# Kernel optimization log

Measured on AMD Instinct MI355X. Metric: run time of the kernel, lower is better.

The kernel has to match this reference:

```python
import jax, jax.numpy as jnp
import numpy as np

VOCAB = 25
HIDDEN = 512
B, S = 64, 2048


def setup_inputs() -> dict:
    key = jax.random.key(0)
    ks = jax.random.split(key, 8)
    tokens = jax.random.randint(ks[0], (B, S), 0, VOCAB)
    lengths = jax.random.randint(ks[1], (B,), 1, S + 1)  # pack_padded requires length >= 1
    k = 1.0 / np.sqrt(HIDDEN)
    u = lambda kk, shp: jax.random.uniform(kk, shp, jnp.float32, -k, k)
    return {
        "tokens": tokens,
        "lengths": lengths,
        "W_ih": u(ks[2], (4 * HIDDEN, VOCAB)),   # gate order i,f,g,o (PyTorch)
        "W_hh": u(ks[3], (4 * HIDDEN, HIDDEN)),
        "b_ih": u(ks[4], (4 * HIDDEN,)),
        "b_hh": u(ks[5], (4 * HIDDEN,)),
        "fc_w": u(ks[6], (1, HIDDEN)),
        "fc_b": u(ks[7], (1,)),
    }


def _lstm_last_hidden(x, lengths, W_ih, W_hh, b_ih, b_hh):
    # x: [B,S,V] one-hot; returns h at each sequence's last valid step (packed-LSTM semantics)
    b, s, _ = x.shape
    h0 = jnp.zeros((b, HIDDEN), x.dtype)
    c0 = jnp.zeros((b, HIDDEN), x.dtype)
    # precompute input projections for all steps: [S,B,4H]
    xg = jnp.einsum('bsv,gv->sbg', x, W_ih) + b_ih + b_hh

    def step(carry, inp):
        h, c = carry
        xt, t = inp
        gates = xt + h @ W_hh.T
        i, f, g, o = jnp.split(gates, 4, axis=-1)
        i = jax.nn.sigmoid(i); f = jax.nn.sigmoid(f)
        g = jnp.tanh(g); o = jax.nn.sigmoid(o)
        c_new = f * c + i * g
        h_new = o * jnp.tanh(c_new)
        m = (t < lengths)[:, None]  # freeze state past sequence end
        return (jnp.where(m, h_new, h), jnp.where(m, c_new, c)), None

    (h, _), _ = jax.lax.scan(step, (h0, c0), (xg, jnp.arange(s)))
    return h


def reference(tokens, lengths, W_ih, W_hh, b_ih, b_hh, fc_w, fc_b):
    # sort by length descending, like the torch forward (output stays in sorted order)
    order = jnp.argsort(-lengths)
    toks = tokens[order]
    lens = lengths[order]
    x = jax.nn.one_hot(toks, VOCAB, dtype=jnp.float32)  # fused one-hot (replaces python loop)
    h = _lstm_last_hidden(x, lens, W_ih, W_hh, b_ih, b_hh)
    return h @ fc_w.T + fc_b  # [B,1]
```

## Files before the change

### kernel.cpp

```cpp
#include <hip/hip_runtime.h>


#define VOCAB 25
#define HIDDEN 512
#define BATCH 64
#define SEQ 2048
#define GB 16
#define NG 4
#define WPG 16
#define HSL 32
#define RWG 128
#define NTHREADS 256
#define HGQ (GB * HIDDEN / 2)

typedef short s16x8 __attribute__((ext_vector_type(8)));
typedef float f32x4 __attribute__((ext_vector_type(4)));

__device__ inline unsigned short f2bf(float x) {
  unsigned u = __float_as_uint(x);
  u += 0x7fffu + ((u >> 16) & 1u);
  return (unsigned short)(u >> 16);
}
__device__ inline float sigf(float x) { return 1.0f / (1.0f + __expf(-x)); }
__device__ inline float tanh_fast(float x) { return 2.0f / (1.0f + __expf(-2.0f * x)) - 1.0f; }

__global__ void prep_kernel(unsigned long long* hg, float* out) {
  const int i = blockIdx.x * blockDim.x + threadIdx.x;
  const int n = blockDim.x * gridDim.x;
  for (int k = i; k < 2 * NG * HGQ; k += n) hg[k] = 0ull;
  if (i < BATCH) out[i] = 0.f;
}

__global__ __launch_bounds__(NTHREADS, 1) void lstm_persistent(
    const int* __restrict__ tokens, const int* __restrict__ lengths,
    const float* __restrict__ W_ih, const float* __restrict__ W_hh,
    const float* __restrict__ b_ih, const float* __restrict__ b_hh,
    const float* __restrict__ fc_w, const float* __restrict__ fc_b,
    float* __restrict__ out, unsigned long long* hg) {
  const int tid = threadIdx.x;
  const int bid = blockIdx.x;
  const int x = bid & 7;
  const int g = x >> 1;
  const int w = ((bid >> 3) << 1) | (x & 1);

  __shared__ __align__(16) unsigned short hbuf[GB][HIDDEN + 8];
  __shared__ float gatesb[GB][RWG + 5];
  __shared__ float xgt[VOCAB][RWG + 5];
  __shared__ int lenAll[BATCH];
  __shared__ int order_[BATCH];
  __shared__ int gIdx[GB];
  __shared__ int gLen[GB];

  if (tid < BATCH) lenAll[tid] = lengths[tid];
  __syncthreads();
  if (tid < BATCH) {
    const int L = lenAll[tid];
    int r = 0;
    for (int j = 0; j < BATCH; ++j) {
      const int lj = lenAll[j];
      r += ((lj > L) || (lj == L && j < tid)) ? 1 : 0;
    }
    order_[r] = tid;
  }
  __syncthreads();
  if (tid < GB) {
    const int oi = order_[g * GB + tid];
    gIdx[tid] = oi;
    gLen[tid] = lenAll[oi];
  }
  for (int i = tid; i < GB * (HIDDEN + 8); i += NTHREADS)
    ((unsigned short*)hbuf)[i] = 0;
  for (int i = tid; i < VOCAB * RWG; i += NTHREADS) {
    const int v = i / RWG, rl = i % RWG;
    const int rg = (rl >> 5) * HIDDEN + w * HSL + (rl & 31);
    xgt[v][rl] = W_ih[rg * VOCAB + v] + b_ih[rg] + b_hh[rg];
  }
  __syncthreads();

  const int T = gLen[0];
  const int lane = tid & 63;
  const int wv = tid >> 6;
  const int m16 = lane & 15;
  const int quad = lane >> 4;

  s16x8 Bf[2][16];
#pragma unroll
  for (int nti = 0; nti < 2; ++nti) {
    const int nt = wv + 4 * nti;
    const int rl = nt * 16 + m16;
    const int rg = (rl >> 5) * HIDDEN + w * HSL + (rl & 31);
    const float* wr = W_hh + (size_t)rg * HIDDEN;
#pragma unroll
    for (int kt = 0; kt < 16; ++kt) {
      const float* p = wr + kt * 32 + quad * 8;
#pragma unroll
      for (int e = 0; e < 8; ++e) Bf[nti][kt][e] = (short)f2bf(p[e]);
    }
  }

  const int cb = tid >> 4;
  const int cs = tid & 15;
  const int jj0 = 2 * cs, jj1 = 2 * cs + 1;
  const int myLen = gLen[cb];
  const int* tokRow = tokens + (size_t)gIdx[cb] * SEQ;
  unsigned long long* const base0 = hg + (size_t)g * HGQ;
  unsigned long long* const base1 = hg + (size_t)(NG + g) * HGQ;

  float c0 = 0.f, c1 = 0.f, h0 = 0.f, h1 = 0.f;

  for (int t = 0; t < T; ++t) {
    const int tok = tokRow[t];

    if (t > 0) {
      const unsigned long long* src = ((t & 1) ? base1 : base0) + tid;
      unsigned long long q[16];
      for (;;) {
        bool ok = true;
#pragma unroll
        for (int r = 0; r < 16; ++r)
          q[r] = __hip_atomic_load(src + r * 256, __ATOMIC_RELAXED,
                                   __HIP_MEMORY_SCOPE_AGENT);
#pragma unroll
        for (int r = 0; r < 16; ++r) ok &= ((unsigned)(q[r] >> 32) == (unsigned)t);
        if (ok) break;
      }
#pragma unroll
      for (int r = 0; r < 16; ++r)
        *(unsigned*)&hbuf[cb][r * 32 + jj0] = (unsigned)q[r];
    }
    __syncthreads();

    f32x4 acc0a = {0.f, 0.f, 0.f, 0.f}, acc0b = {0.f, 0.f, 0.f, 0.f};
    f32x4 acc1a = {0.f, 0.f, 0.f, 0.f}, acc1b = {0.f, 0.f, 0.f, 0.f};
#pragma unroll
    for (int kt = 0; kt < 16; kt += 2) {
      const s16x8 A0 = *(const s16x8*)&hbuf[m16][kt * 32 + quad * 8];
      const s16x8 A1 = *(const s16x8*)&hbuf[m16][(kt + 1) * 32 + quad * 8];
      acc0a = __builtin_amdgcn_mfma_f32_16x16x32_bf16(A0, Bf[0][kt], acc0a, 0, 0, 0);
      acc1a = __builtin_amdgcn_mfma_f32_16x16x32_bf16(A0, Bf[1][kt], acc1a, 0, 0, 0);
      acc0b = __builtin_amdgcn_mfma_f32_16x16x32_bf16(A1, Bf[0][kt + 1], acc0b, 0, 0, 0);
      acc1b = __builtin_amdgcn_mfma_f32_16x16x32_bf16(A1, Bf[1][kt + 1], acc1b, 0, 0, 0);
    }
    const f32x4 acc0 = acc0a + acc0b;
    const f32x4 acc1 = acc1a + acc1b;
#pragma unroll
    for (int v = 0; v < 4; ++v) {
      gatesb[quad * 4 + v][wv * 16 + m16] = acc0[v];
      gatesb[quad * 4 + v][(wv + 4) * 16 + m16] = acc1[v];
    }
    __syncthreads();

    const float pi0 = gatesb[cb][jj0] + xgt[tok][jj0];
    const float pf0 = gatesb[cb][32 + jj0] + xgt[tok][32 + jj0];
    const float pg0 = gatesb[cb][64 + jj0] + xgt[tok][64 + jj0];
    const float po0 = gatesb[cb][96 + jj0] + xgt[tok][96 + jj0];
    const float pi1 = gatesb[cb][jj1] + xgt[tok][jj1];
    const float pf1 = gatesb[cb][32 + jj1] + xgt[tok][32 + jj1];
    const float pg1 = gatesb[cb][64 + jj1] + xgt[tok][64 + jj1];
    const float po1 = gatesb[cb][96 + jj1] + xgt[tok][96 + jj1];
    if (t < myLen) {
      const float i0 = sigf(pi0), f0 = sigf(pf0), g0 = tanh_fast(pg0), o0 = sigf(po0);
      c0 = f0 * c0 + i0 * g0;
      h0 = o0 * tanh_fast(c0);
      const float i1 = sigf(pi1), f1 = sigf(pf1), g1 = tanh_fast(pg1), o1 = sigf(po1);
      c1 = f1 * c1 + i1 * g1;
      h1 = o1 * tanh_fast(c1);
    }
    if (t + 1 < T) {
      const unsigned payload = (unsigned)f2bf(h0) | ((unsigned)f2bf(h1) << 16);
      const unsigned long long qv = ((unsigned long long)(unsigned)(t + 1) << 32) | payload;
      unsigned long long* hp = (((t + 1) & 1) ? base1 : base0) + w * 256 + tid;
      __hip_atomic_store(hp, qv, __ATOMIC_RELAXED, __HIP_MEMORY_SCOPE_AGENT);
    }
  }

  float part = h0 * fc_w[w * HSL + jj0] + h1 * fc_w[w * HSL + jj1];
  part += __shfl_down(part, 8, 16);
  part += __shfl_down(part, 4, 16);
  part += __shfl_down(part, 2, 16);
  part += __shfl_down(part, 1, 16);
  if (cs == 0) {
    if (w == 0) part += fc_b[0];
    atomicAdd(&out[g * GB + cb], part);
  }
}

extern "C" void kernel_launch(void* const* d_in, const int* in_sizes, int n_in,
                              void* d_out, int out_size, void* d_ws, size_t ws_size,
                              hipStream_t stream) {
  (void)in_sizes; (void)n_in; (void)out_size; (void)ws_size;
  const int* tokens = (const int*)d_in[0];
  const int* lengths = (const int*)d_in[1];
  const float* W_ih = (const float*)d_in[2];
  const float* W_hh = (const float*)d_in[3];
  const float* b_ih = (const float*)d_in[4];
  const float* b_hh = (const float*)d_in[5];
  const float* fc_w = (const float*)d_in[6];
  const float* fc_b = (const float*)d_in[7];
  float* out = (float*)d_out;
  unsigned long long* hglob = (unsigned long long*)d_ws;

  prep_kernel<<<32, 256, 0, stream>>>(hglob, out);
  lstm_persistent<<<64, NTHREADS, 0, stream>>>(tokens, lengths, W_ih, W_hh, b_ih, b_hh,
                                               fc_w, fc_b, out, hglob);
}
```

Baseline: 5.560 ms.

## Split each batch group into two interleaved half-groups to overlap exchange latency

Each block's 16-sequence group is split into two 8-sequence subgroups (P and Q, alternating by length rank), which are processed alternately within each timestep. While one subgroup computes, the other's hidden-state exchange is issued early through inline-asm global loads, hiding cross-block synchronisation latency. The exchange format packs a 16-bit tag with each bf16 value, halving the payload per word. The MFMA tiles are now half empty (only 8 of 16 rows are valid), and the extra __syncthreads and the more complex tag polling add overhead.

```diff
diff --git a/kernel.cpp b/kernel.cpp
--- a/kernel.cpp
+++ b/kernel.cpp
@@ -5,16 +5,16 @@
 #define HIDDEN 512
 #define BATCH 64
 #define SEQ 2048
-#define GB 16
-#define NG 4
+#define GBH 8
 #define WPG 16
 #define HSL 32
 #define RWG 128
 #define NTHREADS 256
-#define HGQ (GB * HIDDEN / 2)
+#define GQW 2048
 
 typedef short s16x8 __attribute__((ext_vector_type(8)));
 typedef float f32x4 __attribute__((ext_vector_type(4)));
+typedef unsigned long long ull;
 
 __device__ inline unsigned short f2bf(float x) {
   unsigned u = __float_as_uint(x);
@@ -24,10 +24,35 @@
 __device__ inline float sigf(float x) { return 1.0f / (1.0f + __expf(-x)); }
 __device__ inline float tanh_fast(float x) { return 2.0f / (1.0f + __expf(-2.0f * x)) - 1.0f; }
 
-__global__ void prep_kernel(unsigned long long* hg, float* out) {
+#define PREFETCH8(QARR, QB)                                                  \
+  asm volatile(                                                              \
+      "global_load_dwordx2 %[a0], %[v0], %[b] sc0 sc1\n\t"                   \
+      "global_load_dwordx2 %[a1], %[v0], %[b] offset:1024 sc0 sc1\n\t"       \
+      "global_load_dwordx2 %[a2], %[v0], %[b] offset:2048 sc0 sc1\n\t"       \
+      "global_load_dwordx2 %[a3], %[v0], %[b] offset:3072 sc0 sc1\n\t"       \
+      "global_load_dwordx2 %[a4], %[v1], %[b] sc0 sc1\n\t"                   \
+      "global_load_dwordx2 %[a5], %[v1], %[b] offset:1024 sc0 sc1\n\t"       \
+      "global_load_dwordx2 %[a6], %[v1], %[b] offset:2048 sc0 sc1\n\t"       \
+      "global_load_dwordx2 %[a7], %[v1], %[b] offset:3072 sc0 sc1"           \
+      : [a0] "=&v"(QARR[0]), [a1] "=&v"(QARR[1]), [a2] "=&v"(QARR[2]),       \
+        [a3] "=&v"(QARR[3]), [a4] "=&v"(QARR[4]), [a5] "=&v"(QARR[5]),       \
+        [a6] "=&v"(QARR[6]), [a7] "=&v"(QARR[7])                             \
+      : [v0] "v"(vo0), [v1] "v"(vo1), [b] "s"(QB)                            \
+      : "memory")
+
+#define TAGOK8(QARR, TU, OK)                                                 \
+  do {                                                                       \
+    OK = true;                                                               \
+    _Pragma("unroll") for (int r_ = 0; r_ < 8; ++r_) {                       \
+      OK &= (((unsigned)(QARR[r_] >> 16) & 0xFFFFu) == (TU));                \
+      OK &= (((unsigned)(QARR[r_] >> 48)) == (TU));                          \
+    }                                                                        \
+  } while (0)
+
+__global__ void prep_kernel(ull* hg, float* out) {
   const int i = blockIdx.x * blockDim.x + threadIdx.x;
   const int n = blockDim.x * gridDim.x;
-  for (int k = i; k < 2 * NG * HGQ; k += n) hg[k] = 0ull;
+  for (int k = i; k < 16 * GQW; k += n) hg[k] = 0ull;
   if (i < BATCH) out[i] = 0.f;
 }
 
@@ -36,40 +61,44 @@
     const float* __restrict__ W_ih, const float* __restrict__ W_hh,
     const float* __restrict__ b_ih, const float* __restrict__ b_hh,
     const float* __restrict__ fc_w, const float* __restrict__ fc_b,
-    float* __restrict__ out, unsigned long long* hg) {
+    float* __restrict__ out, ull* hg) {
   const int tid = threadIdx.x;
   const int bid = blockIdx.x;
-  const int x = bid & 7;
-  const int g = x >> 1;
-  const int w = ((bid >> 3) << 1) | (x & 1);
-
-  __shared__ __align__(16) unsigned short hbuf[GB][HIDDEN + 8];
-  __shared__ float gatesb[GB][RWG + 5];
+  const int xr = bid & 7;
+  const int pair = xr >> 1;
+  const int w = ((bid >> 3) << 1) | (xr & 1);
+
+  __shared__ __align__(16) unsigned short hbufP[16][HIDDEN + 8];
+  __shared__ __align__(16) unsigned short hbufQ[16][HIDDEN + 8];
+  __shared__ float gatesbP[GBH][RWG + 5];
+  __shared__ float gatesbQ[GBH][RWG + 5];
   __shared__ float xgt[VOCAB][RWG + 5];
   __shared__ int lenAll[BATCH];
   __shared__ int order_[BATCH];
-  __shared__ int gIdx[GB];
-  __shared__ int gLen[GB];
+  __shared__ int gIdxP[GBH], gLenP[GBH], gIdxQ[GBH], gLenQ[GBH];
 
   if (tid < BATCH) lenAll[tid] = lengths[tid];
   __syncthreads();
   if (tid < BATCH) {
     const int L = lenAll[tid];
     int r = 0;
-    for (int j = 0; j < BATCH; ++j) {
-      const int lj = lenAll[j];
-      r += ((lj > L) || (lj == L && j < tid)) ? 1 : 0;
+    for (int jx = 0; jx < BATCH; ++jx) {
+      const int lj = lenAll[jx];
+      r += ((lj > L) || (lj == L && jx < tid)) ? 1 : 0;
     }
     order_[r] = tid;
   }
   __syncthreads();
-  if (tid < GB) {
-    const int oi = order_[g * GB + tid];
-    gIdx[tid] = oi;
-    gLen[tid] = lenAll[oi];
-  }
-  for (int i = tid; i < GB * (HIDDEN + 8); i += NTHREADS)
-    ((unsigned short*)hbuf)[i] = 0;
+  if (tid < GBH) {
+    const int rp = pair * 16 + 2 * tid;
+    const int op = order_[rp], oq = order_[rp + 1];
+    gIdxP[tid] = op; gLenP[tid] = lenAll[op];
+    gIdxQ[tid] = oq; gLenQ[tid] = lenAll[oq];
+  }
+  for (int i = tid; i < 16 * (HIDDEN + 8); i += NTHREADS) {
+    ((unsigned short*)hbufP)[i] = 0;
+    ((unsigned short*)hbufQ)[i] = 0;
+  }
   for (int i = tid; i < VOCAB * RWG; i += NTHREADS) {
     const int v = i / RWG, rl = i % RWG;
     const int rg = (rl >> 5) * HIDDEN + w * HSL + (rl & 31);
@@ -77,7 +106,8 @@
   }
   __syncthreads();
 
-  const int T = gLen[0];
+  const int TP = gLenP[0];
+  const int TQ = gLenQ[0];
   const int lane = tid & 63;
   const int wv = tid >> 6;
   const int m16 = lane & 15;
@@ -98,90 +128,197 @@
     }
   }
 
-  const int cb = tid >> 4;
-  const int cs = tid & 15;
-  const int jj0 = 2 * cs, jj1 = 2 * cs + 1;
-  const int myLen = gLen[cb];
-  const int* tokRow = tokens + (size_t)gIdx[cb] * SEQ;
-  unsigned long long* const base0 = hg + (size_t)g * HGQ;
-  unsigned long long* const base1 = hg + (size_t)(NG + g) * HGQ;
-
-  float c0 = 0.f, c1 = 0.f, h0 = 0.f, h1 = 0.f;
-
-  for (int t = 0; t < T; ++t) {
-    const int tok = tokRow[t];
+  const int cb = tid >> 5;
+  const int j = tid & 31;
+  const int h128 = tid >> 7;
+  const int cbq = (tid >> 4) & 7;
+  const int pp = tid & 15;
+  const int myLenP = gLenP[cb], myLenQ = gLenQ[cb];
+  const int* tokRowP = tokens + (size_t)gIdxP[cb] * SEQ;
+  const int* tokRowQ = tokens + (size_t)gIdxQ[cb] * SEQ;
+
+  ull* const bP0 = hg + (size_t)(2 * pair) * GQW;
+  ull* const bP1 = hg + (size_t)(8 + 2 * pair) * GQW;
+  ull* const bQ0 = hg + (size_t)(2 * pair + 1) * GQW;
+  ull* const bQ1 = hg + (size_t)(8 + 2 * pair + 1) * GQW;
+
+  const unsigned vo0 = (unsigned)(h128 * 8192 + (cbq * 16 + pp) * 8);
+  const unsigned vo1 = vo0 + 4096;
+  const int sIdx = w * 256 + cb * 32 + j;
+
+  ull qP[8], qQ[8];
+  float cP = 0.f, hP = 0.f, cQ = 0.f, hQ = 0.f;
+
+  for (int t = 0; t < TP; ++t) {
+    const unsigned tu = (unsigned)t;
 
     if (t > 0) {
-      const unsigned long long* src = ((t & 1) ? base1 : base0) + tid;
-      unsigned long long q[16];
-      for (;;) {
-        bool ok = true;
-#pragma unroll
-        for (int r = 0; r < 16; ++r)
-          q[r] = __hip_atomic_load(src + r * 256, __ATOMIC_RELAXED,
-                                   __HIP_MEMORY_SCOPE_AGENT);
-#pragma unroll
-        for (int r = 0; r < 16; ++r) ok &= ((unsigned)(q[r] >> 32) == (unsigned)t);
-        if (ok) break;
-      }
-#pragma unroll
-      for (int r = 0; r < 16; ++r)
-        *(unsigned*)&hbuf[cb][r * 32 + jj0] = (unsigned)q[r];
+      asm volatile("s_waitcnt vmcnt(1)" ::: "memory");
+      __builtin_amdgcn_sched_barrier(0);
+      bool ok;
+      TAGOK8(qP, tu, ok);
+      if (!ok) {
+        const ull* src = ((t & 1) ? bP1 : bP0) + h128 * 1024 + cbq * 16 + pp;
+        for (;;) {
+#pragma unroll
+          for (int r = 0; r < 8; ++r)
+            qP[r] = __hip_atomic_load(src + r * 128, __ATOMIC_RELAXED,
+                                      __HIP_MEMORY_SCOPE_AGENT);
+          TAGOK8(qP, tu, ok);
+          if (ok) break;
+        }
+      }
+#pragma unroll
+      for (int r = 0; r < 8; ++r) {
+        const unsigned lo = (unsigned)qP[r] & 0xFFFFu;
+        const unsigned hi = (unsigned)(qP[r] >> 32) & 0xFFFFu;
+        *(unsigned*)&hbufP[cbq][(h128 * 8 + r) * 32 + 2 * pp] = lo | (hi << 16);
+      }
     }
     __syncthreads();
-
-    f32x4 acc0a = {0.f, 0.f, 0.f, 0.f}, acc0b = {0.f, 0.f, 0.f, 0.f};
-    f32x4 acc1a = {0.f, 0.f, 0.f, 0.f}, acc1b = {0.f, 0.f, 0.f, 0.f};
-#pragma unroll
-    for (int kt = 0; kt < 16; kt += 2) {
-      const s16x8 A0 = *(const s16x8*)&hbuf[m16][kt * 32 + quad * 8];
-      const s16x8 A1 = *(const s16x8*)&hbuf[m16][(kt + 1) * 32 + quad * 8];
-      acc0a = __builtin_amdgcn_mfma_f32_16x16x32_bf16(A0, Bf[0][kt], acc0a, 0, 0, 0);
-      acc1a = __builtin_amdgcn_mfma_f32_16x16x32_bf16(A0, Bf[1][kt], acc1a, 0, 0, 0);
-      acc0b = __builtin_amdgcn_mfma_f32_16x16x32_bf16(A1, Bf[0][kt + 1], acc0b, 0, 0, 0);
-      acc1b = __builtin_amdgcn_mfma_f32_16x16x32_bf16(A1, Bf[1][kt + 1], acc1b, 0, 0, 0);
-    }
-    const f32x4 acc0 = acc0a + acc0b;
-    const f32x4 acc1 = acc1a + acc1b;
-#pragma unroll
-    for (int v = 0; v < 4; ++v) {
-      gatesb[quad * 4 + v][wv * 16 + m16] = acc0[v];
-      gatesb[quad * 4 + v][(wv + 4) * 16 + m16] = acc1[v];
+    const int tokP = tokRowP[t];
+    {
+      f32x4 a0a = {0.f,0.f,0.f,0.f}, a0b = {0.f,0.f,0.f,0.f};
+      f32x4 a1a = {0.f,0.f,0.f,0.f}, a1b = {0.f,0.f,0.f,0.f};
+#pragma unroll
+      for (int kt = 0; kt < 16; kt += 2) {
+        const s16x8 A0 = *(const s16x8*)&hbufP[m16][kt * 32 + quad * 8];
+        const s16x8 A1 = *(const s16x8*)&hbufP[m16][(kt + 1) * 32 + quad * 8];
+        a0a = __builtin_amdgcn_mfma_f32_16x16x32_bf16(A0, Bf[0][kt], a0a, 0, 0, 0);
+        a1a = __builtin_amdgcn_mfma_f32_16x16x32_bf16(A0, Bf[1][kt], a1a, 0, 0, 0);
+        a0b = __builtin_amdgcn_mfma_f32_16x16x32_bf16(A1, Bf[0][kt + 1], a0b, 0, 0, 0);
+        a1b = __builtin_amdgcn_mfma_f32_16x16x32_bf16(A1, Bf[1][kt + 1], a1b, 0, 0, 0);
+      }
+      const f32x4 ac0 = a0a + a0b, ac1 = a1a + a1b;
+      if (quad < 2) {
+#pragma unroll
+        for (int v = 0; v < 4; ++v) {
+          gatesbP[quad * 4 + v][wv * 16 + m16] = ac0[v];
+          gatesbP[quad * 4 + v][(wv + 4) * 16 + m16] = ac1[v];
+        }
+      }
     }
     __syncthreads();
-
-    const float pi0 = gatesb[cb][jj0] + xgt[tok][jj0];
-    const float pf0 = gatesb[cb][32 + jj0] + xgt[tok][32 + jj0];
-    const float pg0 = gatesb[cb][64 + jj0] + xgt[tok][64 + jj0];
-    const float po0 = gatesb[cb][96 + jj0] + xgt[tok][96 + jj0];
-    const float pi1 = gatesb[cb][jj1] + xgt[tok][jj1];
-    const float pf1 = gatesb[cb][32 + jj1] + xgt[tok][32 + jj1];
-    const float pg1 = gatesb[cb][64 + jj1] + xgt[tok][64 + jj1];
-    const float po1 = gatesb[cb][96 + jj1] + xgt[tok][96 + jj1];
-    if (t < myLen) {
-      const float i0 = sigf(pi0), f0 = sigf(pf0), g0 = tanh_fast(pg0), o0 = sigf(po0);
-      c0 = f0 * c0 + i0 * g0;
-      h0 = o0 * tanh_fast(c0);
-      const float i1 = sigf(pi1), f1 = sigf(pf1), g1 = tanh_fast(pg1), o1 = sigf(po1);
-      c1 = f1 * c1 + i1 * g1;
-      h1 = o1 * tanh_fast(c1);
-    }
-    if (t + 1 < T) {
-      const unsigned payload = (unsigned)f2bf(h0) | ((unsigned)f2bf(h1) << 16);
-      const unsigned long long qv = ((unsigned long long)(unsigned)(t + 1) << 32) | payload;
-      unsigned long long* hp = (((t + 1) & 1) ? base1 : base0) + w * 256 + tid;
-      __hip_atomic_store(hp, qv, __ATOMIC_RELAXED, __HIP_MEMORY_SCOPE_AGENT);
-    }
-  }
-
-  float part = h0 * fc_w[w * HSL + jj0] + h1 * fc_w[w * HSL + jj1];
-  part += __shfl_down(part, 8, 16);
-  part += __shfl_down(part, 4, 16);
-  part += __shfl_down(part, 2, 16);
-  part += __shfl_down(part, 1, 16);
-  if (cs == 0) {
-    if (w == 0) part += fc_b[0];
-    atomicAdd(&out[g * GB + cb], part);
+    if (t > 0 && t < TQ) {
+      const ull* qb = (t & 1) ? bQ1 : bQ0;
+      PREFETCH8(qQ, qb);
+    }
+    {
+      const float pi = gatesbP[cb][j] + xgt[tokP][j];
+      const float pf = gatesbP[cb][32 + j] + xgt[tokP][32 + j];
+      const float pg = gatesbP[cb][64 + j] + xgt[tokP][64 + j];
+      const float po = gatesbP[cb][96 + j] + xgt[tokP][96 + j];
+      if (t < myLenP) {
+        const float ii = sigf(pi), ff = sigf(pf), gg = tanh_fast(pg), oo = sigf(po);
+        cP = ff * cP + ii * gg;
+        hP = oo * tanh_fast(cP);
+      }
+      if (t + 1 < TP) {
+        unsigned* dst = (unsigned*)(((t + 1) & 1) ? bP1 : bP0) + sIdx;
+        __hip_atomic_store(dst, ((unsigned)(t + 1) << 16) | (unsigned)f2bf(hP),
+                           __ATOMIC_RELAXED, __HIP_MEMORY_SCOPE_AGENT);
+      }
+    }
+
+    if (t < TQ) {
+      if (t > 0) {
+        asm volatile("s_waitcnt vmcnt(1)" ::: "memory");
+        __builtin_amdgcn_sched_barrier(0);
+        bool ok;
+        TAGOK8(qQ, tu, ok);
+        if (!ok) {
+          const ull* src = ((t & 1) ? bQ1 : bQ0) + h128 * 1024 + cbq * 16 + pp;
+          for (;;) {
+#pragma unroll
+            for (int r = 0; r < 8; ++r)
+              qQ[r] = __hip_atomic_load(src + r * 128, __ATOMIC_RELAXED,
+                                        __HIP_MEMORY_SCOPE_AGENT);
+            TAGOK8(qQ, tu, ok);
+            if (ok) break;
+          }
+        }
+#pragma unroll
+        for (int r = 0; r < 8; ++r) {
+          const unsigned lo = (unsigned)qQ[r] & 0xFFFFu;
+          const unsigned hi = (unsigned)(qQ[r] >> 32) & 0xFFFFu;
+          *(unsigned*)&hbufQ[cbq][(h128 * 8 + r) * 32 + 2 * pp] = lo | (hi << 16);
+        }
+      }
+      __syncthreads();
+      const int tokQ = tokRowQ[t];
+      {
+        f32x4 a0a = {0.f,0.f,0.f,0.f}, a0b = {0.f,0.f,0.f,0.f};
+        f32x4 a1a = {0.f,0.f,0.f,0.f}, a1b = {0.f,0.f,0.f,0.f};
+#pragma unroll
+        for (int kt = 0; kt < 16; kt += 2) {
+          const s16x8 A0 = *(const s16x8*)&hbufQ[m16][kt * 32 + quad * 8];
+          const s16x8 A1 = *(const s16x8*)&hbufQ[m16][(kt + 1) * 32 + quad * 8];
+          a0a = __builtin_amdgcn_mfma_f32_16x16x32_bf16(A0, Bf[0][kt], a0a, 0, 0, 0);
+          a1a = __builtin_amdgcn_mfma_f32_16x16x32_bf16(A0, Bf[1][kt], a1a, 0, 0, 0);
+          a0b = __builtin_amdgcn_mfma_f32_16x16x32_bf16(A1, Bf[0][kt + 1], a0b, 0, 0, 0);
+          a1b = __builtin_amdgcn_mfma_f32_16x16x32_bf16(A1, Bf[1][kt + 1], a1b, 0, 0, 0);
+        }
+        const f32x4 ac0 = a0a + a0b, ac1 = a1a + a1b;
+        if (quad < 2) {
+#pragma unroll
+          for (int v = 0; v < 4; ++v) {
+            gatesbQ[quad * 4 + v][wv * 16 + m16] = ac0[v];
+            gatesbQ[quad * 4 + v][(wv + 4) * 16 + m16] = ac1[v];
+          }
+        }
+      }
+      __syncthreads();
+      if (t + 1 < TP) {
+        const ull* qb = ((t + 1) & 1) ? bP1 : bP0;
+        PREFETCH8(qP, qb);
+      }
+      {
+        const float pi = gatesbQ[cb][j] + xgt[tokQ][j];
+        const float pf = gatesbQ[cb][32 + j] + xgt[tokQ][32 + j];
+        const float pg = gatesbQ[cb][64 + j] + xgt[tokQ][64 + j];
+        const float po = gatesbQ[cb][96 + j] + xgt[tokQ][96 + j];
+        if (t < myLenQ) {
+          const float ii = sigf(pi), ff = sigf(pf), gg = tanh_fast(pg), oo = sigf(po);
+          cQ = ff * cQ + ii * gg;
+          hQ = oo * tanh_fast(cQ);
+        }
+        if (t + 1 < TQ) {
+          unsigned* dst = (unsigned*)(((t + 1) & 1) ? bQ1 : bQ0) + sIdx;
+          __hip_atomic_store(dst, ((unsigned)(t + 1) << 16) | (unsigned)f2bf(hQ),
+                             __ATOMIC_RELAXED, __HIP_MEMORY_SCOPE_AGENT);
+        }
+      }
+    } else {
+      if (t + 1 < TP) {
+        const ull* qb = ((t + 1) & 1) ? bP1 : bP0;
+        PREFETCH8(qP, qb);
+      }
+    }
+  }
+
+  {
+    float part = hP * fc_w[w * HSL + j];
+    part += __shfl_down(part, 16, 32);
+    part += __shfl_down(part, 8, 32);
+    part += __shfl_down(part, 4, 32);
+    part += __shfl_down(part, 2, 32);
+    part += __shfl_down(part, 1, 32);
+    if (j == 0) {
+      if (w == 0) part += fc_b[0];
+      atomicAdd(&out[pair * 16 + 2 * cb], part);
+    }
+  }
+  {
+    float part = hQ * fc_w[w * HSL + j];
+    part += __shfl_down(part, 16, 32);
+    part += __shfl_down(part, 8, 32);
+    part += __shfl_down(part, 4, 32);
+    part += __shfl_down(part, 2, 32);
+    part += __shfl_down(part, 1, 32);
+    if (j == 0) {
+      if (w == 0) part += fc_b[0];
+      atomicAdd(&out[pair * 16 + 2 * cb + 1], part);
+    }
   }
 }
 
@@ -198,7 +335,7 @@
   const float* fc_w = (const float*)d_in[6];
   const float* fc_b = (const float*)d_in[7];
   float* out = (float*)d_out;
-  unsigned long long* hglob = (unsigned long long*)d_ws;
+  ull* hglob = (ull*)d_ws;
 
   prep_kernel<<<32, 256, 0, stream>>>(hglob, out);
   lstm_persistent<<<64, NTHREADS, 0, stream>>>(tokens, lengths, W_ih, W_hh, b_ih, b_hh,
```

Result: slower. 6.893 ms (+24.0%).

## Split each batch group into four sub-batches and pipeline the hidden-state exchange

Applied to the files above, without the earlier changes.

Each 16-sequence group is split into four sub-batches of four sequences, processed round-robin within a timestep. While one sub-batch computes, the hidden-state exchange loads for another sub-batch are issued early through inline-asm global loads, to hide the inter-block communication latency. Sub-batches also stop once their own maximum length is reached, and the exchange packs a 16-bit step tag with each bf16 value in 32-bit words. The cost is four MFMA passes that each use only four of sixteen rows, plus roughly four times as many block barriers per step.

```diff
diff --git a/kernel.cpp b/kernel.cpp
--- a/kernel.cpp
+++ b/kernel.cpp
@@ -5,16 +5,16 @@
 #define HIDDEN 512
 #define BATCH 64
 #define SEQ 2048
-#define GB 16
-#define NG 4
-#define WPG 16
+#define NSETS 4
 #define HSL 32
 #define RWG 128
 #define NTHREADS 256
-#define HGQ (GB * HIDDEN / 2)
+#define GDW 2048
 
 typedef short s16x8 __attribute__((ext_vector_type(8)));
 typedef float f32x4 __attribute__((ext_vector_type(4)));
+typedef unsigned long long ull;
+typedef unsigned short ushort_t;
 
 __device__ inline unsigned short f2bf(float x) {
   unsigned u = __float_as_uint(x);
@@ -24,11 +24,11 @@
 __device__ inline float sigf(float x) { return 1.0f / (1.0f + __expf(-x)); }
 __device__ inline float tanh_fast(float x) { return 2.0f / (1.0f + __expf(-2.0f * x)) - 1.0f; }
 
-__global__ void prep_kernel(unsigned long long* hg, float* out) {
-  const int i = blockIdx.x * blockDim.x + threadIdx.x;
+__global__ void prep_kernel(unsigned* hg, float* out) {
+  const int i0 = blockIdx.x * blockDim.x + threadIdx.x;
   const int n = blockDim.x * gridDim.x;
-  for (int k = i; k < 2 * NG * HGQ; k += n) hg[k] = 0ull;
-  if (i < BATCH) out[i] = 0.f;
+  for (int k = i0; k < 2 * NSETS * 4 * GDW; k += n) hg[k] = 0u;
+  if (i0 < BATCH) out[i0] = 0.f;
 }
 
 __global__ __launch_bounds__(NTHREADS, 1) void lstm_persistent(
@@ -36,40 +36,40 @@
     const float* __restrict__ W_ih, const float* __restrict__ W_hh,
     const float* __restrict__ b_ih, const float* __restrict__ b_hh,
     const float* __restrict__ fc_w, const float* __restrict__ fc_b,
-    float* __restrict__ out, unsigned long long* hg) {
+    float* __restrict__ out, unsigned* hg) {
   const int tid = threadIdx.x;
   const int bid = blockIdx.x;
   const int x = bid & 7;
-  const int g = x >> 1;
+  const int s = x >> 1;
   const int w = ((bid >> 3) << 1) | (x & 1);
 
-  __shared__ __align__(16) unsigned short hbuf[GB][HIDDEN + 8];
-  __shared__ float gatesb[GB][RWG + 5];
+  __shared__ __align__(16) ushort_t hbuf[4][16][HIDDEN + 8];
+  __shared__ float gatesb[4][4][RWG + 5];
   __shared__ float xgt[VOCAB][RWG + 5];
   __shared__ int lenAll[BATCH];
   __shared__ int order_[BATCH];
-  __shared__ int gIdx[GB];
-  __shared__ int gLen[GB];
+  __shared__ int gIdxS[16];
+  __shared__ int gLenS[16];
 
   if (tid < BATCH) lenAll[tid] = lengths[tid];
   __syncthreads();
   if (tid < BATCH) {
     const int L = lenAll[tid];
     int r = 0;
-    for (int j = 0; j < BATCH; ++j) {
-      const int lj = lenAll[j];
-      r += ((lj > L) || (lj == L && j < tid)) ? 1 : 0;
+    for (int jx = 0; jx < BATCH; ++jx) {
+      const int lj = lenAll[jx];
+      r += ((lj > L) || (lj == L && jx < tid)) ? 1 : 0;
     }
     order_[r] = tid;
   }
   __syncthreads();
-  if (tid < GB) {
-    const int oi = order_[g * GB + tid];
-    gIdx[tid] = oi;
-    gLen[tid] = lenAll[oi];
-  }
-  for (int i = tid; i < GB * (HIDDEN + 8); i += NTHREADS)
-    ((unsigned short*)hbuf)[i] = 0;
+  if (tid < 16) {
+    const int oi = order_[s * 16 + tid];
+    gIdxS[tid] = oi;
+    gLenS[tid] = lenAll[oi];
+  }
+  for (int i = tid; i < 4 * 16 * (HIDDEN + 8); i += NTHREADS)
+    ((ushort_t*)hbuf)[i] = 0;
   for (int i = tid; i < VOCAB * RWG; i += NTHREADS) {
     const int v = i / RWG, rl = i % RWG;
     const int rg = (rl >> 5) * HIDDEN + w * HSL + (rl & 31);
@@ -77,7 +77,11 @@
   }
   __syncthreads();
 
-  const int T = gLen[0];
+  int TGa[4];
+#pragma unroll
+  for (int i = 0; i < 4; ++i) TGa[i] = gLenS[i];
+  const int T = TGa[0];
+
   const int lane = tid & 63;
   const int wv = tid >> 6;
   const int m16 = lane & 15;
@@ -98,90 +102,139 @@
     }
   }
 
-  const int cb = tid >> 4;
-  const int cs = tid & 15;
-  const int jj0 = 2 * cs, jj1 = 2 * cs + 1;
-  const int myLen = gLen[cb];
-  const int* tokRow = tokens + (size_t)gIdx[cb] * SEQ;
-  unsigned long long* const base0 = hg + (size_t)g * HGQ;
-  unsigned long long* const base1 = hg + (size_t)(NG + g) * HGQ;
-
-  float c0 = 0.f, c1 = 0.f, h0 = 0.f, h1 = 0.f;
+  const int cb = (tid >> 5) & 3;
+  const int j = tid & 31;
+  const bool cellTh = tid < 128;
+  const int* tokR[4];
+  int myLen[4];
+#pragma unroll
+  for (int i = 0; i < 4; ++i) {
+    const int lr = 4 * cb + i;
+    const int gi = gIdxS[lr];
+    tokR[i] = tokens + (size_t)gi * SEQ;
+    myLen[i] = gLenS[lr];
+  }
+
+  ull qG[4][4];
+  float cS[4] = {0.f, 0.f, 0.f, 0.f};
+  float hS[4] = {0.f, 0.f, 0.f, 0.f};
+  const unsigned voA = (unsigned)(tid * 8);
+  const unsigned voB = voA + 4096u;
 
   for (int t = 0; t < T; ++t) {
-    const int tok = tokRow[t];
-
-    if (t > 0) {
-      const unsigned long long* src = ((t & 1) ? base1 : base0) + tid;
-      unsigned long long q[16];
-      for (;;) {
-        bool ok = true;
-#pragma unroll
-        for (int r = 0; r < 16; ++r)
-          q[r] = __hip_atomic_load(src + r * 256, __ATOMIC_RELAXED,
-                                   __HIP_MEMORY_SCOPE_AGENT);
-#pragma unroll
-        for (int r = 0; r < 16; ++r) ok &= ((unsigned)(q[r] >> 32) == (unsigned)t);
-        if (ok) break;
+    const unsigned tu = (unsigned)t;
+#pragma unroll
+    for (int i = 0; i < 4; ++i) {
+      const bool alive = (t < TGa[i]);
+      if (alive) {
+        if (t > 0) {
+          asm volatile("s_waitcnt vmcnt(0)" ::: "memory");
+          __builtin_amdgcn_sched_barrier(0);
+          bool ok = true;
+#pragma unroll
+          for (int r = 0; r < 4; ++r) {
+            ok &= (((unsigned)(qG[i][r] >> 16) & 0xFFFFu) == tu);
+            ok &= (((unsigned)(qG[i][r] >> 48)) == tu);
+          }
+          if (!ok) {
+            const ull* src =
+                (const ull*)(hg + (size_t)(((t & 1) * NSETS + s) * 4 + i) * GDW) + tid;
+            for (;;) {
+#pragma unroll
+              for (int r = 0; r < 4; ++r)
+                qG[i][r] = __hip_atomic_load(src + r * 256, __ATOMIC_RELAXED,
+                                             __HIP_MEMORY_SCOPE_AGENT);
+              ok = true;
+#pragma unroll
+              for (int r = 0; r < 4; ++r) {
+                ok &= (((unsigned)(qG[i][r] >> 16) & 0xFFFFu) == tu);
+                ok &= (((unsigned)(qG[i][r] >> 48)) == tu);
+              }
+              if (ok) break;
+            }
+          }
+#pragma unroll
+          for (int r = 0; r < 4; ++r) {
+            const int d0 = 2 * (tid + 256 * r);
+            const int wsrc = d0 >> 7;
+            const int bq = (d0 >> 5) & 3;
+            const int ju = d0 & 31;
+            const unsigned lo = (unsigned)qG[i][r] & 0xFFFFu;
+            const unsigned hi = (unsigned)(qG[i][r] >> 32) & 0xFFFFu;
+            *(unsigned*)&hbuf[i][bq][wsrc * 32 + ju] = lo | (hi << 16);
+          }
+        }
+        __syncthreads();
+        f32x4 a0a = {0.f, 0.f, 0.f, 0.f}, a0b = {0.f, 0.f, 0.f, 0.f};
+        f32x4 a1a = {0.f, 0.f, 0.f, 0.f}, a1b = {0.f, 0.f, 0.f, 0.f};
+#pragma unroll
+        for (int kt = 0; kt < 16; kt += 2) {
+          const s16x8 A0 = *(const s16x8*)&hbuf[i][m16][kt * 32 + quad * 8];
+          const s16x8 A1 = *(const s16x8*)&hbuf[i][m16][(kt + 1) * 32 + quad * 8];
+          a0a = __builtin_amdgcn_mfma_f32_16x16x32_bf16(A0, Bf[0][kt], a0a, 0, 0, 0);
+          a1a = __builtin_amdgcn_mfma_f32_16x16x32_bf16(A0, Bf[1][kt], a1a, 0, 0, 0);
+          a0b = __builtin_amdgcn_mfma_f32_16x16x32_bf16(A1, Bf[0][kt + 1], a0b, 0, 0, 0);
+          a1b = __builtin_amdgcn_mfma_f32_16x16x32_bf16(A1, Bf[1][kt + 1], a1b, 0, 0, 0);
+        }
+        const f32x4 ac0 = a0a + a0b, ac1 = a1a + a1b;
+        if (quad == 0) {
+#pragma unroll
+          for (int v = 0; v < 4; ++v) {
+            gatesb[i][v][wv * 16 + m16] = ac0[v];
+            gatesb[i][v][(wv + 4) * 16 + m16] = ac1[v];
+          }
+        }
+        __syncthreads();
       }
-#pragma unroll
-      for (int r = 0; r < 16; ++r)
-        *(unsigned*)&hbuf[cb][r * 32 + jj0] = (unsigned)q[r];
-    }
-    __syncthreads();
-
-    f32x4 acc0a = {0.f, 0.f, 0.f, 0.f}, acc0b = {0.f, 0.f, 0.f, 0.f};
-    f32x4 acc1a = {0.f, 0.f, 0.f, 0.f}, acc1b = {0.f, 0.f, 0.f, 0.f};
-#pragma unroll
-    for (int kt = 0; kt < 16; kt += 2) {
-      const s16x8 A0 = *(const s16x8*)&hbuf[m16][kt * 32 + quad * 8];
-      const s16x8 A1 = *(const s16x8*)&hbuf[m16][(kt + 1) * 32 + quad * 8];
-      acc0a = __builtin_amdgcn_mfma_f32_16x16x32_bf16(A0, Bf[0][kt], acc0a, 0, 0, 0);
-      acc1a = __builtin_amdgcn_mfma_f32_16x16x32_bf16(A0, Bf[1][kt], acc1a, 0, 0, 0);
-      acc0b = __builtin_amdgcn_mfma_f32_16x16x32_bf16(A1, Bf[0][kt + 1], acc0b, 0, 0, 0);
-      acc1b = __builtin_amdgcn_mfma_f32_16x16x32_bf16(A1, Bf[1][kt + 1], acc1b, 0, 0, 0);
-    }
-    const f32x4 acc0 = acc0a + acc0b;
-    const f32x4 acc1 = acc1a + acc1b;
-#pragma unroll
-    for (int v = 0; v < 4; ++v) {
-      gatesb[quad * 4 + v][wv * 16 + m16] = acc0[v];
-      gatesb[quad * 4 + v][(wv + 4) * 16 + m16] = acc1[v];
-    }
-    __syncthreads();
-
-    const float pi0 = gatesb[cb][jj0] + xgt[tok][jj0];
-    const float pf0 = gatesb[cb][32 + jj0] + xgt[tok][32 + jj0];
-    const float pg0 = gatesb[cb][64 + jj0] + xgt[tok][64 + jj0];
-    const float po0 = gatesb[cb][96 + jj0] + xgt[tok][96 + jj0];
-    const float pi1 = gatesb[cb][jj1] + xgt[tok][jj1];
-    const float pf1 = gatesb[cb][32 + jj1] + xgt[tok][32 + jj1];
-    const float pg1 = gatesb[cb][64 + jj1] + xgt[tok][64 + jj1];
-    const float po1 = gatesb[cb][96 + jj1] + xgt[tok][96 + jj1];
-    if (t < myLen) {
-      const float i0 = sigf(pi0), f0 = sigf(pf0), g0 = tanh_fast(pg0), o0 = sigf(po0);
-      c0 = f0 * c0 + i0 * g0;
-      h0 = o0 * tanh_fast(c0);
-      const float i1 = sigf(pi1), f1 = sigf(pf1), g1 = tanh_fast(pg1), o1 = sigf(po1);
-      c1 = f1 * c1 + i1 * g1;
-      h1 = o1 * tanh_fast(c1);
-    }
-    if (t + 1 < T) {
-      const unsigned payload = (unsigned)f2bf(h0) | ((unsigned)f2bf(h1) << 16);
-      const unsigned long long qv = ((unsigned long long)(unsigned)(t + 1) << 32) | payload;
-      unsigned long long* hp = (((t + 1) & 1) ? base1 : base0) + w * 256 + tid;
-      __hip_atomic_store(hp, qv, __ATOMIC_RELAXED, __HIP_MEMORY_SCOPE_AGENT);
-    }
-  }
-
-  float part = h0 * fc_w[w * HSL + jj0] + h1 * fc_w[w * HSL + jj1];
-  part += __shfl_down(part, 8, 16);
-  part += __shfl_down(part, 4, 16);
-  part += __shfl_down(part, 2, 16);
-  part += __shfl_down(part, 1, 16);
-  if (cs == 0) {
-    if (w == 0) part += fc_b[0];
-    atomicAdd(&out[g * GB + cb], part);
+      {
+        const int jg = (i + 2) & 3;
+        const int tj = (i >= 2) ? (t + 1) : t;
+        if (tj >= 1 && tj < TGa[jg]) {
+          const unsigned* pb = hg + (size_t)(((tj & 1) * NSETS + s) * 4 + jg) * GDW;
+          asm volatile(
+              "global_load_dwordx2 %[a0], %[vA], %[b] sc0 sc1\n\t"
+              "global_load_dwordx2 %[a1], %[vA], %[b] offset:2048 sc0 sc1\n\t"
+              "global_load_dwordx2 %[a2], %[vB], %[b] sc0 sc1\n\t"
+              "global_load_dwordx2 %[a3], %[vB], %[b] offset:2048 sc0 sc1"
+              : [a0] "=&v"(qG[jg][0]), [a1] "=&v"(qG[jg][1]),
+                [a2] "=&v"(qG[jg][2]), [a3] "=&v"(qG[jg][3])
+              : [vA] "v"(voA), [vB] "v"(voB), [b] "s"(pb)
+              : "memory");
+        }
+      }
+      if (alive && cellTh) {
+        const int tok = tokR[i][t];
+        const float pi = gatesb[i][cb][j] + xgt[tok][j];
+        const float pf = gatesb[i][cb][32 + j] + xgt[tok][32 + j];
+        const float pg = gatesb[i][cb][64 + j] + xgt[tok][64 + j];
+        const float po = gatesb[i][cb][96 + j] + xgt[tok][96 + j];
+        if (t < myLen[i]) {
+          const float ii = sigf(pi), ff = sigf(pf), gg = tanh_fast(pg), oo = sigf(po);
+          cS[i] = ff * cS[i] + ii * gg;
+          hS[i] = oo * tanh_fast(cS[i]);
+        }
+        if (t + 1 < TGa[i]) {
+          unsigned* dst = hg + (size_t)((((t + 1) & 1) * NSETS + s) * 4 + i) * GDW +
+                          w * 128 + cb * 32 + j;
+          __hip_atomic_store(dst, ((unsigned)(t + 1) << 16) | (unsigned)f2bf(hS[i]),
+                             __ATOMIC_RELAXED, __HIP_MEMORY_SCOPE_AGENT);
+        }
+      }
+    }
+  }
+
+#pragma unroll
+  for (int i = 0; i < 4; ++i) {
+    float part = cellTh ? hS[i] * fc_w[w * HSL + j] : 0.f;
+    part += __shfl_down(part, 16, 32);
+    part += __shfl_down(part, 8, 32);
+    part += __shfl_down(part, 4, 32);
+    part += __shfl_down(part, 2, 32);
+    part += __shfl_down(part, 1, 32);
+    if (cellTh && j == 0) {
+      if (w == 0) part += fc_b[0];
+      atomicAdd(&out[s * 16 + 4 * cb + i], part);
+    }
   }
 }
 
@@ -198,7 +251,7 @@
   const float* fc_w = (const float*)d_in[6];
   const float* fc_b = (const float*)d_in[7];
   float* out = (float*)d_out;
-  unsigned long long* hglob = (unsigned long long*)d_ws;
+  unsigned* hglob = (unsigned*)d_ws;
 
   prep_kernel<<<32, 256, 0, stream>>>(hglob, out);
   lstm_persistent<<<64, NTHREADS, 0, stream>>>(tokens, lengths, W_ih, W_hh, b_ih, b_hh,
```

After: 12.51 ms. 2.25x slower.
